# Optimization experiments

Measured on AMD Instinct MI355X. Metric: run time of the kernel, lower is better.

Reference implementation:

```python
import jax, jax.numpy as jnp
import numpy as np

EMBED_DIM = 1024
NUM_HEADS = 16
HEAD_DIM = EMBED_DIM // NUM_HEADS
SCALE = HEAD_DIM ** -0.5


def setup_inputs() -> dict:
    key = jax.random.key(0)
    ks = jax.random.split(key, 11)
    B, T, C = 4, 2048, EMBED_DIM
    s = 1.0 / np.sqrt(C)
    return {
        "query": jax.random.normal(ks[0], (B, T, C), jnp.float32),
        "key": jax.random.normal(ks[1], (B, T, C), jnp.float32),
        "value": jax.random.normal(ks[2], (B, T, C), jnp.float32),
        "Wq": jax.random.normal(ks[3], (C, C), jnp.float32) * s,
        "bq": jnp.zeros((C,), jnp.float32),
        "Wk": jax.random.normal(ks[4], (C, C), jnp.float32) * s,
        "bk": jnp.zeros((C,), jnp.float32),
        "Wv": jax.random.normal(ks[5], (C, C), jnp.float32) * s,
        "bv": jnp.zeros((C,), jnp.float32),
        "Wo": jax.random.normal(ks[6], (C, C), jnp.float32) * s,
        "bo": jnp.zeros((C,), jnp.float32),
    }


def reference(query, key, value, Wq, bq, Wk, bk, Wv, bv, Wo, bo):
    B, Tq, C = query.shape
    Tk = key.shape[1]
    H, D = NUM_HEADS, HEAD_DIM
    # Linear projections (torch Linear: x @ W.T + b), split heads -> (B, H, T, D)
    q = (query @ Wq.T + bq).reshape(B, Tq, H, D).transpose(0, 2, 1, 3)
    k = (key @ Wk.T + bk).reshape(B, Tk, H, D).transpose(0, 2, 1, 3)
    v = (value @ Wv.T + bv).reshape(B, Tk, H, D).transpose(0, 2, 1, 3)
    scores = jnp.einsum("bhqd,bhkd->bhqk", q, k) * SCALE
    attn = jax.nn.softmax(scores, axis=-1)
    out = jnp.einsum("bhqk,bhkd->bhqd", attn, v)
    out = out.transpose(0, 2, 1, 3).reshape(B, Tq, C)
    return out @ Wo.T + bo
```

## Files before the change

kernel.cpp:

```cpp
#include <hip/hip_runtime.h>
#include <stdint.h>
#include <math.h>

#define C_DIM 1024
#define H_NUM 16
#define D_DIM 64
#define B_NUM 4
#define T_SEQ 2048
#define M_ROWS (B_NUM * T_SEQ)

#define SCALE_LOG2E (0.125f * 1.44269504088896340736f)

typedef __attribute__((ext_vector_type(8))) __bf16 bf16x8;
typedef __attribute__((ext_vector_type(2))) __bf16 bf16x2;
typedef __attribute__((ext_vector_type(4))) float f32x4;

__device__ __forceinline__ unsigned short f2bf(float f) {
  union { float f; uint32_t u; } v; v.f = f;
  uint32_t r = v.u + 0x7FFFu + ((v.u >> 16) & 1u);
  return (unsigned short)(r >> 16);
}

__device__ __forceinline__ uint32_t pk2bf(float a, float b) {
#if __has_builtin(__builtin_amdgcn_cvt_pk_bf16_f32)
  union { bf16x2 v; uint32_t u; } u;
  u.v = __builtin_amdgcn_cvt_pk_bf16_f32(a, b);
  return u.u;
#else
  union { float f; uint32_t u; } x, y; x.f = a; y.f = b;
  return __builtin_amdgcn_perm(y.u + 0x8000u, x.u + 0x8000u, 0x07060302u);
#endif
}

__device__ __forceinline__ float frcp(float x) {
#if __has_builtin(__builtin_amdgcn_rcpf)
  return __builtin_amdgcn_rcpf(x);
#else
  return 1.f / x;
#endif
}

__device__ __forceinline__ f32x4 mfma16(bf16x8 a, bf16x8 b, f32x4 c) {
  return __builtin_amdgcn_mfma_f32_16x16x32_bf16(a, b, c, 0, 0, 0);
}

__device__ __forceinline__ void cp16(const void* g, void* l) {
  __builtin_amdgcn_global_load_lds(
      (const __attribute__((address_space(1))) unsigned int*)g,
      (__attribute__((address_space(3))) unsigned int*)l, 16, 0, 0);
}

__global__ __launch_bounds__(256) void cast_all(
    const float* __restrict__ a0, const float* __restrict__ a1,
    const float* __restrict__ a2, const float* __restrict__ w0,
    const float* __restrict__ w1, const float* __restrict__ w2,
    const float* __restrict__ w3, unsigned short* __restrict__ oa0,
    unsigned short* __restrict__ oa1, unsigned short* __restrict__ oa2,
    unsigned short* __restrict__ ow0, unsigned short* __restrict__ ow1,
    unsigned short* __restrict__ ow2, unsigned short* __restrict__ ow3,
    int big4, int small4) {
  int i = blockIdx.x * 256 + threadIdx.x;
  int y = blockIdx.y;
  const float* s;
  unsigned short* d;
  int n4;
  switch (y) {
    case 0: s = a0; d = oa0; n4 = big4; break;
    case 1: s = a1; d = oa1; n4 = big4; break;
    case 2: s = a2; d = oa2; n4 = big4; break;
    case 3: s = w0; d = ow0; n4 = small4; break;
    case 4: s = w1; d = ow1; n4 = small4; break;
    case 5: s = w2; d = ow2; n4 = small4; break;
    default: s = w3; d = ow3; n4 = small4; break;
  }
  if (i >= n4) return;
  float4 v = ((const float4*)s)[i];
  ushort4 o;
  o.x = f2bf(v.x); o.y = f2bf(v.y); o.z = f2bf(v.z); o.w = f2bf(v.w);
  ((ushort4*)d)[i] = o;
}

__device__ __forceinline__ void gemm_tile_128(
    const unsigned short* __restrict__ A, const unsigned short* __restrict__ Bw,
    int row0, int col0, unsigned short* As, unsigned short* Bs, f32x4 acc[4][4]) {
  const int lane = threadIdx.x & 63;
  const int wave = threadIdx.x >> 6;
  const int wm = wave >> 1, wn = wave & 1;
#pragma unroll
  for (int mt = 0; mt < 4; ++mt)
#pragma unroll
    for (int nt = 0; nt < 4; ++nt) acc[mt][nt] = (f32x4){0.f, 0.f, 0.f, 0.f};

#define GQSTAGE(kk, bb)                                                        \
  {                                                                            \
    _Pragma("unroll") for (int rr = 0; rr < 4; ++rr) {                         \
      int c = (rr * 4 + wave) * 64 + lane;                                     \
      int row = c >> 3;                                                        \
      int g = (c & 7) ^ (row & 7);                                             \
      cp16(A + (size_t)(row0 + row) * C_DIM + (kk) + g * 8,                    \
           As + (bb) * 8192 + (rr * 4 + wave) * 512);                          \
      cp16(Bw + (size_t)(col0 + row) * C_DIM + (kk) + g * 8,                   \
           Bs + (bb) * 8192 + (rr * 4 + wave) * 512);                          \
    }                                                                          \
  }

  GQSTAGE(0, 0);
  for (int it = 0; it < C_DIM / 64; ++it) {
    const int buf = it & 1;
    __syncthreads();
    if (it + 1 < C_DIM / 64) GQSTAGE((it + 1) * 64, buf ^ 1);
    const unsigned short* Ab = As + buf * 8192;
    const unsigned short* Bb = Bs + buf * 8192;
#pragma unroll
    for (int ks = 0; ks < 2; ++ks) {
      bf16x8 af[4], bfr[4];
#pragma unroll
      for (int mt = 0; mt < 4; ++mt) {
        int row = wm * 64 + mt * 16 + (lane & 15);
        int gs = (ks * 4 + (lane >> 4)) ^ (row & 7);
        af[mt] = *(const bf16x8*)(Ab + row * 64 + gs * 8);
      }
#pragma unroll
      for (int nt = 0; nt < 4; ++nt) {
        int row = wn * 64 + nt * 16 + (lane & 15);
        int gs = (ks * 4 + (lane >> 4)) ^ (row & 7);
        bfr[nt] = *(const bf16x8*)(Bb + row * 64 + gs * 8);
      }
#pragma unroll
      for (int mt = 0; mt < 4; ++mt)
#pragma unroll
        for (int nt = 0; nt < 4; ++nt)
          acc[mt][nt] = mfma16(af[mt], bfr[nt], acc[mt][nt]);
    }
  }
#undef GQSTAGE
}

__global__ __launch_bounds__(256) void gemm_qkv(
    const unsigned short* __restrict__ qb, const unsigned short* __restrict__ kb,
    const unsigned short* __restrict__ vb, const unsigned short* __restrict__ wq,
    const unsigned short* __restrict__ wk, const unsigned short* __restrict__ wv,
    const float* __restrict__ bq, const float* __restrict__ bk,
    const float* __restrict__ bv, unsigned short* __restrict__ Qp,
    unsigned short* __restrict__ Kp, unsigned short* __restrict__ Vp) {
  __shared__ alignas(16) unsigned short As[2][128 * 64];
  __shared__ alignas(16) unsigned short Bs[2][128 * 64];
  const int lin = blockIdx.x + 8 * blockIdx.y + 512 * blockIdx.z;
  const int rowb = ((lin & 7) << 3) | ((lin >> 3) & 7);
  const int colb = (lin >> 6) & 7;
  const int z = lin >> 9;
  const unsigned short* A = (z == 0) ? qb : (z == 1) ? kb : vb;
  const unsigned short* W = (z == 0) ? wq : (z == 1) ? wk : wv;
  const float* bias = (z == 0) ? bq : (z == 1) ? bk : bv;
  const int m0 = rowb * 128, n0 = colb * 128;

  const int lane = threadIdx.x & 63;
  const int wave = threadIdx.x >> 6;
  const int wm = wave >> 1, wn = wave & 1;
  const int quad = lane >> 4;
  const int q15 = lane & 15;
  f32x4 acc[4][4];

  if (z == 2) {
    gemm_tile_128(A, W, m0, n0, &As[0][0], &Bs[0][0], acc);
#pragma unroll
    for (int mt = 0; mt < 4; ++mt)
#pragma unroll
      for (int nt = 0; nt < 4; ++nt) {
        int n = n0 + wn * 64 + nt * 16 + q15;
        float bval = bias[n];
        int h = n >> 6, d = n & 63;
        int m0t = m0 + wm * 64 + mt * 16 + quad * 4;
        int b = m0t >> 11, t0 = m0t & 2047;
        float f0 = acc[mt][nt][0] + bval, f1 = acc[mt][nt][1] + bval;
        float f2 = acc[mt][nt][2] + bval, f3 = acc[mt][nt][3] + bval;
        uint2 pk = {pk2bf(f0, f1), pk2bf(f2, f3)};
        size_t off = (((size_t)(b * H_NUM + h) * (T_SEQ / 8) + (t0 >> 3)) * D_DIM + d) * 8
                     + (t0 & 7);
        *(uint2*)(Vp + off) = pk;
      }
  } else {
    gemm_tile_128(W, A, n0, m0, &As[0][0], &Bs[0][0], acc);
    unsigned short* dst = (z == 0) ? Qp : Kp;
    const float sc = (z == 0) ? SCALE_LOG2E : 1.0f;
#pragma unroll
    for (int mt = 0; mt < 4; ++mt) {
      int nb = n0 + wm * 64 + mt * 16 + quad * 4;
      float4 b4 = *(const float4*)(bias + nb);
      int h = nb >> 6, d0 = nb & 63;
#pragma unroll
      for (int nt = 0; nt < 4; ++nt) {
        int m = m0 + wn * 64 + nt * 16 + q15;
        int b = m >> 11, t = m & 2047;
        float f0 = (acc[mt][nt][0] + b4.x) * sc;
        float f1 = (acc[mt][nt][1] + b4.y) * sc;
        float f2 = (acc[mt][nt][2] + b4.z) * sc;
        float f3 = (acc[mt][nt][3] + b4.w) * sc;
        uint2 pk = {pk2bf(f0, f1), pk2bf(f2, f3)};
        *(uint2*)(dst + ((size_t)(b * H_NUM + h) * T_SEQ + t) * D_DIM + d0) = pk;
      }
    }
  }
}

__device__ __forceinline__ int fsw(int r) { return (r + ((r >> 3) << 2)) & 7; }

__global__ __launch_bounds__(256, 3) void attn_kernel(
    const unsigned short* __restrict__ Qp, const unsigned short* __restrict__ Kp,
    const unsigned short* __restrict__ Vp, unsigned short* __restrict__ Op) {
  __shared__ alignas(16) unsigned short Ks[2][64 * 64];
  __shared__ alignas(16) unsigned short Vt[2][64 * 64];
  const int bh = blockIdx.x;
  const int q0 = blockIdx.y * 128;
  const int lane = threadIdx.x & 63;
  const int wave = threadIdx.x >> 6;
  const int quad = lane >> 4;
  const int q15 = lane & 15;

  bf16x8 qf[2][2];
#pragma unroll
  for (int g = 0; g < 2; ++g) {
    const unsigned short* qrow =
        Qp + ((size_t)bh * T_SEQ + q0 + wave * 32 + g * 16 + q15) * D_DIM;
    qf[g][0] = *(const bf16x8*)(qrow + quad * 8);
    qf[g][1] = *(const bf16x8*)(qrow + 32 + quad * 8);
  }

  bf16x8 onesf;
#pragma unroll
  for (int i = 0; i < 8; ++i) onesf[i] = (__bf16)1.0f;

  f32x4 oacc[2][4];
  f32x4 lacc[2];
#pragma unroll
  for (int g = 0; g < 2; ++g) {
    lacc[g] = (f32x4){0.f, 0.f, 0.f, 0.f};
#pragma unroll
    for (int dt = 0; dt < 4; ++dt) oacc[g][dt] = (f32x4){0.f, 0.f, 0.f, 0.f};
  }

  const unsigned short* Kbase = Kp + (size_t)bh * T_SEQ * D_DIM;
  const unsigned short* Vbase = Vp + (size_t)bh * T_SEQ * D_DIM;

#define STAGE(kt, buf)                                                        \
  {                                                                           \
    _Pragma("unroll") for (int i = 0; i < 2; ++i) {                           \
      int chunk = wave * 2 + i;                                     \
      int c = chunk * 64 + lane;                                              \
      int row = c >> 3;                                                       \
      int g = (c & 7) ^ fsw(row);                                             \
      cp16(Kbase + ((size_t)((kt) * 64 + row)) * D_DIM + g * 8,               \
           &Ks[buf][chunk * 512]);                                            \
      cp16(Vbase + (size_t)((kt) * 8 + chunk) * 512 + lane * 8,               \
           &Vt[buf][chunk * 512]);                                            \
    }                                                                         \
  }

  STAGE(0, 0);

  for (int kt = 0; kt < T_SEQ / 64; ++kt) {
    const int buf = kt & 1;
    __syncthreads();
    if (kt + 1 < T_SEQ / 64) STAGE(kt + 1, buf ^ 1);

    bf16x8 kfr[4][2];
#pragma unroll
    for (int mt = 0; mt < 4; ++mt) {
      int rowp = 32 * (mt >> 1) + (q15 >> 2) * 8 + (mt & 1) * 4 + (q15 & 3);
#pragma unroll
      for (int ks = 0; ks < 2; ++ks) {
        int gs = (ks * 4 + quad) ^ fsw(rowp);
        kfr[mt][ks] = *(const bf16x8*)(&Ks[buf][rowp * 64 + gs * 8]);
      }
    }
    bf16x8 Pb[2][2];
#pragma unroll
    for (int g = 0; g < 2; ++g) {
      f32x4 s[4];
#pragma unroll
      for (int mt = 0; mt < 4; ++mt) s[mt] = (f32x4){0.f, 0.f, 0.f, 0.f};
#pragma unroll
      for (int ks = 0; ks < 2; ++ks)
#pragma unroll
        for (int mt = 0; mt < 4; ++mt)
          s[mt] = mfma16(kfr[mt][ks], qf[g][ks], s[mt]);
#pragma unroll
      for (int a = 0; a < 2; ++a) {
        float p0 = __builtin_amdgcn_exp2f(s[2 * a][0]);
        float p1 = __builtin_amdgcn_exp2f(s[2 * a][1]);
        float p2 = __builtin_amdgcn_exp2f(s[2 * a][2]);
        float p3 = __builtin_amdgcn_exp2f(s[2 * a][3]);
        float p4 = __builtin_amdgcn_exp2f(s[2 * a + 1][0]);
        float p5 = __builtin_amdgcn_exp2f(s[2 * a + 1][1]);
        float p6 = __builtin_amdgcn_exp2f(s[2 * a + 1][2]);
        float p7 = __builtin_amdgcn_exp2f(s[2 * a + 1][3]);
        union { bf16x8 v; uint32_t u[4]; } pk;
        pk.u[0] = pk2bf(p0, p1);
        pk.u[1] = pk2bf(p2, p3);
        pk.u[2] = pk2bf(p4, p5);
        pk.u[3] = pk2bf(p6, p7);
        Pb[g][a] = pk.v;
      }
    }

#pragma unroll
    for (int a = 0; a < 2; ++a) {
      lacc[0] = mfma16(onesf, Pb[0][a], lacc[0]);
      lacc[1] = mfma16(onesf, Pb[1][a], lacc[1]);
#pragma unroll
      for (int dt = 0; dt < 4; ++dt) {
        bf16x8 vf =
            *(const bf16x8*)(&Vt[buf][((a * 4 + quad) * 64 + dt * 16 + q15) * 8]);
        oacc[0][dt] = mfma16(vf, Pb[0][a], oacc[0][dt]);
        oacc[1][dt] = mfma16(vf, Pb[1][a], oacc[1][dt]);
      }
    }
  }
#undef STAGE

  const int b = bh >> 4, h = bh & 15;
#pragma unroll
  for (int g = 0; g < 2; ++g) {
    float inv = frcp(lacc[g][0]);
    int t = q0 + wave * 32 + g * 16 + q15;
#pragma unroll
    for (int dt = 0; dt < 4; ++dt) {
      uint2 o = {pk2bf(oacc[g][dt][0] * inv, oacc[g][dt][1] * inv),
                 pk2bf(oacc[g][dt][2] * inv, oacc[g][dt][3] * inv)};
      int col = h * D_DIM + dt * 16 + quad * 4;
      *(uint2*)(Op + ((size_t)b * T_SEQ + t) * C_DIM + col) = o;
    }
  }
}

__global__ __launch_bounds__(256) void gemm_out_kernel(
    const unsigned short* __restrict__ Op, const unsigned short* __restrict__ wo,
    const float* __restrict__ bo, float* __restrict__ out) {
  __shared__ alignas(16) unsigned short As[2][128 * 64];
  __shared__ alignas(16) unsigned short Bs[2][128 * 64];
  const int lin = blockIdx.x + 8 * blockIdx.y;
  const int rowb = ((lin & 7) << 3) | ((lin >> 3) & 7);
  const int colb = (lin >> 6) & 7;
  const int row0 = rowb * 128, col0 = colb * 128;
  f32x4 acc[4][4];
  gemm_tile_128(Op, wo, row0, col0, &As[0][0], &Bs[0][0], acc);

  const int lane = threadIdx.x & 63;
  const int wave = threadIdx.x >> 6;
  const int wm = wave >> 1, wn = wave & 1;
#pragma unroll
  for (int mt = 0; mt < 4; ++mt)
#pragma unroll
    for (int nt = 0; nt < 4; ++nt) {
      int n = col0 + wn * 64 + nt * 16 + (lane & 15);
      float bval = bo[n];
#pragma unroll
      for (int r = 0; r < 4; ++r) {
        int m = row0 + wm * 64 + mt * 16 + (lane >> 4) * 4 + r;
        out[(size_t)m * C_DIM + n] = acc[mt][nt][r] + bval;
      }
    }
}

extern "C" void kernel_launch(void* const* d_in, const int* in_sizes, int n_in,
                              void* d_out, int out_size, void* d_ws, size_t ws_size,
                              hipStream_t stream) {
  const float* q_in = (const float*)d_in[0];
  const float* k_in = (const float*)d_in[1];
  const float* v_in = (const float*)d_in[2];
  const float* Wq = (const float*)d_in[3];
  const float* bq = (const float*)d_in[4];
  const float* Wk = (const float*)d_in[5];
  const float* bk = (const float*)d_in[6];
  const float* Wv = (const float*)d_in[7];
  const float* bv = (const float*)d_in[8];
  const float* Wo = (const float*)d_in[9];
  const float* bo = (const float*)d_in[10];
  float* out = (float*)d_out;

  const size_t MC = (size_t)M_ROWS * C_DIM;
  const size_t CC = (size_t)C_DIM * C_DIM;
  unsigned short* qb = (unsigned short*)d_ws;
  unsigned short* kb = qb + MC;
  unsigned short* vb = kb + MC;
  unsigned short* wqb = vb + MC;
  unsigned short* wkb = wqb + CC;
  unsigned short* wvb = wkb + CC;
  unsigned short* wob = wvb + CC;
  unsigned short* Qp = wob + CC;
  unsigned short* Kp = Qp + MC;
  unsigned short* Vp = Kp + MC;
  unsigned short* Op = Vp + MC;

  const int big4 = (int)(MC / 4), small4 = (int)(CC / 4);
  cast_all<<<dim3((big4 + 255) / 256, 7), dim3(256), 0, stream>>>(
      q_in, k_in, v_in, Wq, Wk, Wv, Wo, qb, kb, vb, wqb, wkb, wvb, wob,
      big4, small4);

  gemm_qkv<<<dim3(C_DIM / 128, M_ROWS / 128, 3), dim3(256), 0, stream>>>(
      qb, kb, vb, wqb, wkb, wvb, bq, bk, bv, Qp, Kp, Vp);

  attn_kernel<<<dim3(B_NUM * H_NUM, T_SEQ / 128), dim3(256), 0, stream>>>(
      Qp, Kp, Vp, Op);

  gemm_out_kernel<<<dim3(C_DIM / 128, M_ROWS / 128), dim3(256), 0, stream>>>(
      Op, wob, bo, out);
}
```

Baseline: 328.1 us.

## Load V fragments directly from global into registers, double-buffered, bypassing LDS

```diff
diff --git a/kernel.cpp b/kernel.cpp
--- a/kernel.cpp
+++ b/kernel.cpp
@@ -209,7 +209,6 @@
     const unsigned short* __restrict__ Qp, const unsigned short* __restrict__ Kp,
     const unsigned short* __restrict__ Vp, unsigned short* __restrict__ Op) {
   __shared__ alignas(16) unsigned short Ks[2][64 * 64];
-  __shared__ alignas(16) unsigned short Vt[2][64 * 64];
   const int bh = blockIdx.x;
   const int q0 = blockIdx.y * 128;
   const int lane = threadIdx.x & 63;
@@ -240,9 +239,10 @@
   }
 
   const unsigned short* Kbase = Kp + (size_t)bh * T_SEQ * D_DIM;
-  const unsigned short* Vbase = Vp + (size_t)bh * T_SEQ * D_DIM;
-
-#define STAGE(kt, buf)                                                        \
+  const unsigned short* Vlane =
+      Vp + (size_t)bh * T_SEQ * D_DIM + quad * 512 + q15 * 8;
+
+#define STAGEK(kt, buf)                                                       \
   {                                                                           \
     _Pragma("unroll") for (int i = 0; i < 2; ++i) {                           \
       int chunk = wave * 2 + i;                                     \
@@ -251,72 +251,74 @@
       int g = (c & 7) ^ fsw(row);                                             \
       cp16(Kbase + ((size_t)((kt) * 64 + row)) * D_DIM + g * 8,               \
            &Ks[buf][chunk * 512]);                                            \
-      cp16(Vbase + (size_t)((kt) * 8 + chunk) * 512 + lane * 8,               \
-           &Vt[buf][chunk * 512]);                                            \
     }                                                                         \
   }
 
-  STAGE(0, 0);
-
-  for (int kt = 0; kt < T_SEQ / 64; ++kt) {
-    const int buf = kt & 1;
-    __syncthreads();
-    if (kt + 1 < T_SEQ / 64) STAGE(kt + 1, buf ^ 1);
-
-    bf16x8 kfr[4][2];
-#pragma unroll
-    for (int mt = 0; mt < 4; ++mt) {
-      int rowp = 32 * (mt >> 1) + (q15 >> 2) * 8 + (mt & 1) * 4 + (q15 & 3);
-#pragma unroll
-      for (int ks = 0; ks < 2; ++ks) {
-        int gs = (ks * 4 + quad) ^ fsw(rowp);
-        kfr[mt][ks] = *(const bf16x8*)(&Ks[buf][rowp * 64 + gs * 8]);
-      }
-    }
-    bf16x8 Pb[2][2];
-#pragma unroll
-    for (int g = 0; g < 2; ++g) {
-      f32x4 s[4];
-#pragma unroll
-      for (int mt = 0; mt < 4; ++mt) s[mt] = (f32x4){0.f, 0.f, 0.f, 0.f};
-#pragma unroll
-      for (int ks = 0; ks < 2; ++ks)
-#pragma unroll
-        for (int mt = 0; mt < 4; ++mt)
-          s[mt] = mfma16(kfr[mt][ks], qf[g][ks], s[mt]);
-#pragma unroll
-      for (int a = 0; a < 2; ++a) {
-        float p0 = __builtin_amdgcn_exp2f(s[2 * a][0]);
-        float p1 = __builtin_amdgcn_exp2f(s[2 * a][1]);
-        float p2 = __builtin_amdgcn_exp2f(s[2 * a][2]);
-        float p3 = __builtin_amdgcn_exp2f(s[2 * a][3]);
-        float p4 = __builtin_amdgcn_exp2f(s[2 * a + 1][0]);
-        float p5 = __builtin_amdgcn_exp2f(s[2 * a + 1][1]);
-        float p6 = __builtin_amdgcn_exp2f(s[2 * a + 1][2]);
-        float p7 = __builtin_amdgcn_exp2f(s[2 * a + 1][3]);
-        union { bf16x8 v; uint32_t u[4]; } pk;
-        pk.u[0] = pk2bf(p0, p1);
-        pk.u[1] = pk2bf(p2, p3);
-        pk.u[2] = pk2bf(p4, p5);
-        pk.u[3] = pk2bf(p6, p7);
-        Pb[g][a] = pk.v;
-      }
-    }
-
-#pragma unroll
-    for (int a = 0; a < 2; ++a) {
-      lacc[0] = mfma16(onesf, Pb[0][a], lacc[0]);
-      lacc[1] = mfma16(onesf, Pb[1][a], lacc[1]);
-#pragma unroll
-      for (int dt = 0; dt < 4; ++dt) {
-        bf16x8 vf =
-            *(const bf16x8*)(&Vt[buf][((a * 4 + quad) * 64 + dt * 16 + q15) * 8]);
-        oacc[0][dt] = mfma16(vf, Pb[0][a], oacc[0][dt]);
-        oacc[1][dt] = mfma16(vf, Pb[1][a], oacc[1][dt]);
-      }
-    }
-  }
-#undef STAGE
+#define ATTN_ITER(kt, buf, VC, VN)                                            \
+  {                                                                           \
+    __syncthreads();                                                          \
+    if ((kt) + 1 < T_SEQ / 64) {                                              \
+      STAGEK((kt) + 1, (buf) ^ 1);                                            \
+      _Pragma("unroll") for (int j = 0; j < 8; ++j)                           \
+          VN[j] = *(const bf16x8*)(Vlane + ((kt) + 1) * 4096 +                \
+                                   (j >> 2) * 2048 + (j & 3) * 128);          \
+    }                                                                         \
+    bf16x8 kfr[4][2];                                                         \
+    _Pragma("unroll") for (int mt = 0; mt < 4; ++mt) {                        \
+      int rowp = 32 * (mt >> 1) + (q15 >> 2) * 8 + (mt & 1) * 4 + (q15 & 3);  \
+      _Pragma("unroll") for (int ks = 0; ks < 2; ++ks) {                      \
+        int gs = (ks * 4 + quad) ^ fsw(rowp);                                 \
+        kfr[mt][ks] = *(const bf16x8*)(&Ks[buf][rowp * 64 + gs * 8]);         \
+      }                                                                       \
+    }                                                                         \
+    bf16x8 Pb[2][2];                                                          \
+    _Pragma("unroll") for (int g = 0; g < 2; ++g) {                           \
+      f32x4 s[4];                                                             \
+      _Pragma("unroll") for (int mt = 0; mt < 4; ++mt)                        \
+          s[mt] = (f32x4){0.f, 0.f, 0.f, 0.f};                                \
+      _Pragma("unroll") for (int ks = 0; ks < 2; ++ks)                        \
+          _Pragma("unroll") for (int mt = 0; mt < 4; ++mt)                    \
+              s[mt] = mfma16(kfr[mt][ks], qf[g][ks], s[mt]);                  \
+      _Pragma("unroll") for (int a = 0; a < 2; ++a) {                         \
+        float p0 = __builtin_amdgcn_exp2f(s[2 * a][0]);                       \
+        float p1 = __builtin_amdgcn_exp2f(s[2 * a][1]);                       \
+        float p2 = __builtin_amdgcn_exp2f(s[2 * a][2]);                       \
+        float p3 = __builtin_amdgcn_exp2f(s[2 * a][3]);                       \
+        float p4 = __builtin_amdgcn_exp2f(s[2 * a + 1][0]);                   \
+        float p5 = __builtin_amdgcn_exp2f(s[2 * a + 1][1]);                   \
+        float p6 = __builtin_amdgcn_exp2f(s[2 * a + 1][2]);                   \
+        float p7 = __builtin_amdgcn_exp2f(s[2 * a + 1][3]);                   \
+        union { bf16x8 v; uint32_t u[4]; } pk;                                \
+        pk.u[0] = pk2bf(p0, p1);                                              \
+        pk.u[1] = pk2bf(p2, p3);                                              \
+        pk.u[2] = pk2bf(p4, p5);                                              \
+        pk.u[3] = pk2bf(p6, p7);                                              \
+        Pb[g][a] = pk.v;                                                      \
+      }                                                                       \
+    }                                                                         \
+    _Pragma("unroll") for (int a = 0; a < 2; ++a) {                           \
+      lacc[0] = mfma16(onesf, Pb[0][a], lacc[0]);                             \
+      lacc[1] = mfma16(onesf, Pb[1][a], lacc[1]);                             \
+      _Pragma("unroll") for (int dt = 0; dt < 4; ++dt) {                      \
+        oacc[0][dt] = mfma16(VC[a * 4 + dt], Pb[0][a], oacc[0][dt]);          \
+        oacc[1][dt] = mfma16(VC[a * 4 + dt], Pb[1][a], oacc[1][dt]);          \
+      }                                                                       \
+    }                                                                         \
+  }
+
+  bf16x8 va[8], vb[8];
+  STAGEK(0, 0);
+#pragma unroll
+  for (int j = 0; j < 8; ++j)
+    va[j] = *(const bf16x8*)(Vlane + (j >> 2) * 2048 + (j & 3) * 128);
+
+#pragma unroll 1
+  for (int kt2 = 0; kt2 < T_SEQ / 128; ++kt2) {
+    ATTN_ITER(kt2 * 2, 0, va, vb);
+    ATTN_ITER(kt2 * 2 + 1, 1, vb, va);
+  }
+#undef ATTN_ITER
+#undef STAGEK
 
   const int b = bh >> 4, h = bh & 15;
 #pragma unroll
```

Result: slower. 385.1 us (+17.4%).
